# Kernel tuning notes

Measured on AMD Instinct MI355X. Metric: run time of the kernel, lower is better.

The kernel has to match this reference:

```python
import jax, jax.numpy as jnp
import numpy as np

EPS = 1e-08

def setup_inputs() -> dict:
    key = jax.random.key(0)
    k1, k2, k3, k4 = jax.random.split(key, 4)
    batch, n_in, n_out, D = 32768, 256, 512, 16
    x = jax.random.uniform(k1, (batch, n_in), jnp.float32, minval=-1.0, maxval=1.0)
    omega = jax.random.normal(k2, (D, 1), jnp.float32)          # stddev=1.0 init
    phase = 0.1 * jax.random.normal(k3, (D, 1), jnp.float32)    # zeros in module; small noise for non-degenerate test
    std_c = 1.0 / np.sqrt(n_in * D)
    c_basis = std_c * jax.random.normal(k4, (n_out, n_in, D), jnp.float32)
    bias = jnp.zeros((n_out,), jnp.float32)
    return {"x": x, "omega": omega, "phase": phase, "c_basis": c_basis, "bias": bias}

def _basis(x, omega, phase):
    # x: (batch, n_in) -> B: (batch, n_in, D)
    D = omega.shape[0]
    w = omega.reshape(1, 1, D)
    p = phase.reshape(1, 1, D)
    wx = w * x[..., None]
    s = jnp.sin(wx + p)
    mu = jnp.exp(-0.5 * w ** 2) * jnp.sin(p)
    std = jnp.sqrt(0.5 * (1.0 - jnp.exp(-2.0 * w ** 2) * jnp.cos(2.0 * p)) - mu ** 2)
    return (s + mu) / (std + EPS)

def reference(x, omega, phase, c_basis, bias):
    B = _basis(x, omega, phase)                     # (batch, n_in, D)
    y = jnp.einsum('bid,oid->bo', B, c_basis)       # (batch, n_out)
    return y + bias
```

## Files before the change

kernel.cpp:

```cpp
#include <hip/hip_runtime.h>
#include <hip/hip_bf16.h>


#define BATCH 32768
#define NIN   256
#define NOUT  512
#define DDIM  16
#define BM    128
#define BN    512
#define BK    64
#define NKT   ((NIN*DDIM)/BK)
#define TILE_BYTES (BN*BK*2)
#define ABYTES (BM*BK*2)
#define BBYTES (BN*BK*2)
#define EPSV  1e-8f
#define INV2PI 0.15915494309189535f

typedef short  bf16x8 __attribute__((ext_vector_type(8)));
typedef float  f32x4  __attribute__((ext_vector_type(4)));

static __device__ __forceinline__ ushort f2bf(float f) {
  union { __hip_bfloat16 h; ushort u; } cv;
  cv.h = __float2bfloat16(f);
  return cv.u;
}

static __device__ __forceinline__ uint cvt_pk(float lo, float hi) {
  uint r;
  asm("v_cvt_pk_bf16_f32 %0, %1, %2" : "=v"(r) : "v"(lo), "v"(hi));
  return r;
}

static __device__ __forceinline__ float sgpr_f(float v) {
  return __builtin_bit_cast(float,
      __builtin_amdgcn_readfirstlane(__builtin_bit_cast(int, v)));
}

__global__ __launch_bounds__(256) void prep_kernel(
    const float* __restrict__ omega, const float* __restrict__ phase,
    const float* __restrict__ c_basis, const float* __restrict__ bias,
    ushort* __restrict__ cb, float* __restrict__ offs)
{
  __shared__ float s_scale[DDIM];
  __shared__ float s_musc[DDIM];
  __shared__ float s_red[4];

  const int o = blockIdx.x;
  const int t = threadIdx.x;

  if (t < DDIM) {
    float w = omega[t];
    float p = phase[t];
    float mu  = expf(-0.5f * w * w) * sinf(p);
    float var = 0.5f * (1.0f - expf(-2.0f * w * w) * cosf(2.0f * p)) - mu * mu;
    float sd  = sqrtf(fmaxf(var, 0.0f));
    float sc  = 1.0f / (sd + EPSV);
    s_scale[t] = sc;
    s_musc[t]  = mu * sc;
  }
  __syncthreads();

  const float* cp = c_basis + ((size_t)o * NIN + t) * DDIM;
  float cv[DDIM];
  {
    const float4* cp4 = (const float4*)cp;
    float4 a = cp4[0], b = cp4[1], c = cp4[2], d = cp4[3];
    cv[0]=a.x; cv[1]=a.y; cv[2]=a.z; cv[3]=a.w;
    cv[4]=b.x; cv[5]=b.y; cv[6]=b.z; cv[7]=b.w;
    cv[8]=c.x; cv[9]=c.y; cv[10]=c.z; cv[11]=c.w;
    cv[12]=d.x; cv[13]=d.y; cv[14]=d.z; cv[15]=d.w;
  }

  float partial = 0.0f;
  uint pk[8];
#pragma unroll
  for (int d = 0; d < DDIM; d += 2) {
    partial += cv[d] * s_musc[d] + cv[d+1] * s_musc[d+1];
    ushort u0 = f2bf(cv[d]   * s_scale[d]);
    ushort u1 = f2bf(cv[d+1] * s_scale[d+1]);
    pk[d >> 1] = (uint)u0 | ((uint)u1 << 16);
  }

  {
    const int r   = o;
    const int kt  = t >> 2;
    const int swz = (r & 7) << 4;
    char* tile = (char*)cb + (size_t)kt * TILE_BYTES;
    int b0 = r * 128 + (t & 3) * 32;
    *(uint4*)(tile + ((b0     ) ^ swz)) = make_uint4(pk[0], pk[1], pk[2], pk[3]);
    *(uint4*)(tile + ((b0 + 16) ^ swz)) = make_uint4(pk[4], pk[5], pk[6], pk[7]);
  }

#pragma unroll
  for (int off = 32; off > 0; off >>= 1) partial += __shfl_down(partial, off, 64);
  if ((t & 63) == 0) s_red[t >> 6] = partial;
  __syncthreads();
  if (t == 0) offs[o] = bias[o] + s_red[0] + s_red[1] + s_red[2] + s_red[3];
}

__global__ __launch_bounds__(512, 2) void gemm_kernel(
    const float* __restrict__ x, const float* __restrict__ omega,
    const float* __restrict__ phase, const ushort* __restrict__ cb,
    const float* __restrict__ offs, float* __restrict__ out)
{
  extern __shared__ char lds[];

  const int t    = threadIdx.x;
  const int lane = t & 63;
  const int wid  = t >> 6;
  const int wm   = wid >> 2;
  const int wn   = wid & 3;
  const int row0 = blockIdx.x * BM;

  float wv[DDIM], pv[DDIM];
#pragma unroll
  for (int d = 0; d < DDIM; ++d) {
    wv[d] = sgpr_f(omega[d] * INV2PI);
    pv[d] = sgpr_f(phase[d] * INV2PI);
  }

  f32x4 acc[4][8];
#pragma unroll
  for (int m = 0; m < 4; ++m)
#pragma unroll
    for (int n = 0; n < 8; ++n) acc[m][n] = (f32x4){0.f, 0.f, 0.f, 0.f};

  const int arow = t >> 2;
  const int acol = t & 3;
  const float* xbase = x + (size_t)(row0 + arow) * NIN + acol;
  const int aswz = (arow & 7) << 4;
  const int ab0  = arow * 128 + acol * 32;

  const int hi  = lane >> 4;
  const int l15 = lane & 15;

#define GLL(s_, d_) __builtin_amdgcn_global_load_lds(                          \
      (const __attribute__((address_space(1))) void*)(s_),                     \
      (__attribute__((address_space(3))) void*)(d_), 16, 0, 0)

#define ISSUE_B(kt_, sb_)                                                      \
  {                                                                            \
    const char* src = (const char*)cb + (size_t)(kt_) * TILE_BYTES             \
                      + wid * 8192 + lane * 16;                                \
    char* dst = lds + 32768 + (sb_) * BBYTES + wid * 8192;                     \
    GLL(src, dst);                 GLL(src + 1024, dst + 1024);                \
    GLL(src + 2048, dst + 2048);   GLL(src + 3072, dst + 3072);                \
    GLL(src + 4096, dst + 4096);   GLL(src + 5120, dst + 5120);                \
    GLL(src + 6144, dst + 6144);   GLL(src + 7168, dst + 7168);                \
  }

#define SINS_ALL(xx_)                                                          \
    _Pragma("unroll")                                                          \
    for (int d = 0; d < DDIM; d += 2) {                                        \
      float s0 = __builtin_amdgcn_sinf(fmaf(wv[d],   (xx_), pv[d]));           \
      float s1 = __builtin_amdgcn_sinf(fmaf(wv[d+1], (xx_), pv[d+1]));         \
      pk[d >> 1] = cvt_pk(s0, s1);                                             \
    }

#define A_WRITE2(sb_)                                                          \
    *(uint4*)(lds + (sb_) * ABYTES + ((ab0     ) ^ aswz)) =                    \
        make_uint4(pk[0], pk[1], pk[2], pk[3]);                                \
    *(uint4*)(lds + (sb_) * ABYTES + ((ab0 + 16) ^ aswz)) =                    \
        make_uint4(pk[4], pk[5], pk[6], pk[7]);

#define MFMA_HALF(mb_, kk_)                                                    \
  {                                                                            \
    const char* AsB = lds + (mb_) * ABYTES;                                    \
    const char* BsB = lds + 32768 + (mb_) * BBYTES;                            \
    bf16x8 af[4];                                                              \
    _Pragma("unroll")                                                          \
    for (int m = 0; m < 4; ++m) {                                              \
      int rr = wm * 64 + m * 16 + l15;                                         \
      af[m] = *(const bf16x8*)(AsB + ((rr*128 + (kk_)*64 + hi*16) ^ ((rr&7)<<4))); \
    }                                                                          \
    __builtin_amdgcn_s_setprio(1);                                             \
    _Pragma("unroll")                                                          \
    for (int nh = 0; nh < 2; ++nh) {                                           \
      bf16x8 bfr[4];                                                           \
      _Pragma("unroll")                                                        \
      for (int n4 = 0; n4 < 4; ++n4) {                                         \
        int rr = wn * 128 + (nh * 4 + n4) * 16 + l15;                          \
        bfr[n4] = *(const bf16x8*)(BsB + ((rr*128 + (kk_)*64 + hi*16) ^ ((rr&7)<<4))); \
      }                                                                        \
      _Pragma("unroll")                                                        \
      for (int m = 0; m < 4; ++m)                                              \
        _Pragma("unroll")                                                      \
        for (int n4 = 0; n4 < 4; ++n4)                                         \
          acc[m][nh * 4 + n4] = __builtin_amdgcn_mfma_f32_16x16x32_bf16(       \
              af[m], bfr[n4], acc[m][nh * 4 + n4], 0, 0, 0);                   \
    }                                                                          \
    __builtin_amdgcn_s_setprio(0);                                             \
  }

#define CBAR(vm_)                                                              \
  __builtin_amdgcn_sched_barrier(0);                                           \
  asm volatile("s_waitcnt vmcnt(" #vm_ ") lgkmcnt(0)" ::: "memory");           \
  __builtin_amdgcn_s_barrier();                                                \
  __builtin_amdgcn_sched_barrier(0);

#define BODY(kt_, mb_, sb_, XU_, XL_)                                          \
  {                                                                            \
    ISSUE_B(((kt_) + 1 < NKT ? (kt_) + 1 : NKT - 1), sb_);                     \
    XL_ = xbase[((kt_) + 2 < NKT ? (kt_) + 2 : NKT - 1) * 4];                  \
    __builtin_amdgcn_sched_barrier(0);                                         \
    MFMA_HALF(mb_, 0)                                                          \
    __builtin_amdgcn_sched_barrier(0);                                         \
    uint pk[8];                                                                \
    SINS_ALL(XU_)                                                              \
    A_WRITE2(sb_)                                                              \
    __builtin_amdgcn_sched_barrier(0);                                         \
    MFMA_HALF(mb_, 1)                                                          \
    CBAR(1)                                                                    \
  }

  float xs0, xs1;
  {
    float xp = xbase[0];
    __builtin_amdgcn_sched_barrier(0);
    ISSUE_B(0, 0);
    __builtin_amdgcn_sched_barrier(0);
    xs1 = xbase[4];
    __builtin_amdgcn_sched_barrier(0);
    {
      uint pk[8];
      SINS_ALL(xp)
      A_WRITE2(0)
    }
    CBAR(1)
  }

  for (int kt = 0; kt < NKT; kt += 2) {
    BODY(kt,     0, 1, xs1, xs0)
    BODY(kt + 1, 1, 0, xs0, xs1)
  }

#pragma unroll
  for (int n = 0; n < 8; ++n) {
    int col = wn * 128 + n * 16 + l15;
    float off = offs[col];
#pragma unroll
    for (int m = 0; m < 4; ++m) {
      int row = row0 + wm * 64 + m * 16 + hi * 4;
      float* op = out + (size_t)row * NOUT + col;
#pragma unroll
      for (int j = 0; j < 4; ++j)
        op[(size_t)j * NOUT] = acc[m][n][j] + off;
    }
  }
}

extern "C" void kernel_launch(void* const* d_in, const int* in_sizes, int n_in,
                              void* d_out, int out_size, void* d_ws, size_t ws_size,
                              hipStream_t stream) {
  const float* x       = (const float*)d_in[0];
  const float* omega   = (const float*)d_in[1];
  const float* phase   = (const float*)d_in[2];
  const float* c_basis = (const float*)d_in[3];
  const float* bias    = (const float*)d_in[4];
  float* out = (float*)d_out;

  float*  offs = (float*)d_ws;
  ushort* cb   = (ushort*)((char*)d_ws + 2048);

  hipFuncSetAttribute((const void*)gemm_kernel,
                      hipFuncAttributeMaxDynamicSharedMemorySize, 163840);

  prep_kernel<<<NOUT, 256, 0, stream>>>(omega, phase, c_basis, bias, cb, offs);
  gemm_kernel<<<BATCH / BM, 512, 163840, stream>>>(x, omega, phase, cb, offs, out);
}
```

Measured before the change: 127.6 us.

## Stagger MFMA and sine phases between wave groups for ping-pong overlap

Splits the main loop body into two variants selected by wave id. One half of the waves runs all MFMAs first and then the sine/A-tile generation, while the other half does the sine work first and then the MFMAs, all between the same barriers. The goal is to have waves on a SIMD alternate between matrix-core work and VALU transcendental work, so both units stay busy rather than every wave fighting for the same one at once. It adds code size and depends on the hardware actually interleaving the two wave groups.

```diff
diff --git a/kernel.cpp b/kernel.cpp
--- a/kernel.cpp
+++ b/kernel.cpp
@@ -192,23 +192,38 @@
     __builtin_amdgcn_s_setprio(0);                                             \
   }
 
+#define SB __builtin_amdgcn_sched_barrier(0);
+
 #define CBAR(vm_)                                                              \
   __builtin_amdgcn_sched_barrier(0);                                           \
   asm volatile("s_waitcnt vmcnt(" #vm_ ") lgkmcnt(0)" ::: "memory");           \
   __builtin_amdgcn_s_barrier();                                                \
   __builtin_amdgcn_sched_barrier(0);
 
-#define BODY(kt_, mb_, sb_, XU_, XL_)                                          \
+#define BODY_A(kt_, mb_, sb_, XU_, XL_)                                        \
   {                                                                            \
     ISSUE_B(((kt_) + 1 < NKT ? (kt_) + 1 : NKT - 1), sb_);                     \
     XL_ = xbase[((kt_) + 2 < NKT ? (kt_) + 2 : NKT - 1) * 4];                  \
-    __builtin_amdgcn_sched_barrier(0);                                         \
+    SB                                                                         \
     MFMA_HALF(mb_, 0)                                                          \
-    __builtin_amdgcn_sched_barrier(0);                                         \
+    MFMA_HALF(mb_, 1)                                                          \
+    SB                                                                         \
     uint pk[8];                                                                \
     SINS_ALL(XU_)                                                              \
     A_WRITE2(sb_)                                                              \
-    __builtin_amdgcn_sched_barrier(0);                                         \
+    CBAR(1)                                                                    \
+  }
+
+#define BODY_B(kt_, mb_, sb_, XU_, XL_)                                        \
+  {                                                                            \
+    ISSUE_B(((kt_) + 1 < NKT ? (kt_) + 1 : NKT - 1), sb_);                     \
+    XL_ = xbase[((kt_) + 2 < NKT ? (kt_) + 2 : NKT - 1) * 4];                  \
+    SB                                                                         \
+    uint pk[8];                                                                \
+    SINS_ALL(XU_)                                                              \
+    A_WRITE2(sb_)                                                              \
+    SB                                                                         \
+    MFMA_HALF(mb_, 0)                                                          \
     MFMA_HALF(mb_, 1)                                                          \
     CBAR(1)                                                                    \
   }
@@ -216,11 +231,11 @@
   float xs0, xs1;
   {
     float xp = xbase[0];
-    __builtin_amdgcn_sched_barrier(0);
+    SB
     ISSUE_B(0, 0);
-    __builtin_amdgcn_sched_barrier(0);
+    SB
     xs1 = xbase[4];
-    __builtin_amdgcn_sched_barrier(0);
+    SB
     {
       uint pk[8];
       SINS_ALL(xp)
@@ -229,9 +244,16 @@
     CBAR(1)
   }
 
-  for (int kt = 0; kt < NKT; kt += 2) {
-    BODY(kt,     0, 1, xs1, xs0)
-    BODY(kt + 1, 1, 0, xs0, xs1)
+  if (wid & 4) {
+    for (int kt = 0; kt < NKT; kt += 2) {
+      BODY_A(kt,     0, 1, xs1, xs0)
+      BODY_A(kt + 1, 1, 0, xs0, xs1)
+    }
+  } else {
+    for (int kt = 0; kt < NKT; kt += 2) {
+      BODY_B(kt,     0, 1, xs1, xs0)
+      BODY_B(kt + 1, 1, 0, xs0, xs1)
+    }
   }
 
 #pragma unroll
```

Result: slower. 143.6 us (+12.5%).

## Switch GEMM to 32x32x16 bf16 MFMA with matching LDS swizzle layout

Applied to the files above, without the earlier changes.

Replaces the 16x16x32 MFMA tiling (4x8 accumulators per wave) with 32x32x16 MFMA (2x4 accumulators), changing fragment loads, the LDS XOR swizzle for both A and the precomputed B tiles, and the output store mapping. Larger MFMA tiles cut the number of LDS fragment reads per FLOP and may suit the matrix core throughput better. The trade-offs are a different bank-conflict pattern from the new swizzle and a less coalesced output store layout.

```diff
diff --git a/kernel.cpp b/kernel.cpp
--- a/kernel.cpp
+++ b/kernel.cpp
@@ -16,8 +16,8 @@
 #define EPSV  1e-8f
 #define INV2PI 0.15915494309189535f
 
-typedef short  bf16x8 __attribute__((ext_vector_type(8)));
-typedef float  f32x4  __attribute__((ext_vector_type(4)));
+typedef short  bf16x8  __attribute__((ext_vector_type(8)));
+typedef float  f32x16  __attribute__((ext_vector_type(16)));
 
 static __device__ __forceinline__ ushort f2bf(float f) {
   union { __hip_bfloat16 h; ushort u; } cv;
@@ -82,13 +82,14 @@
   }
 
   {
-    const int r   = o;
-    const int kt  = t >> 2;
-    const int swz = (r & 7) << 4;
-    char* tile = (char*)cb + (size_t)kt * TILE_BYTES;
-    int b0 = r * 128 + (t & 3) * 32;
-    *(uint4*)(tile + ((b0     ) ^ swz)) = make_uint4(pk[0], pk[1], pk[2], pk[3]);
-    *(uint4*)(tile + ((b0 + 16) ^ swz)) = make_uint4(pk[4], pk[5], pk[6], pk[7]);
+    const int r  = o;
+    const int kt = t >> 2;
+    const int fo = (r >> 2) & 7;
+    char* tile = (char*)cb + (size_t)kt * TILE_BYTES + r * 128;
+    const int u0 = (2 * (t & 3))     ^ fo;
+    const int u1 = (2 * (t & 3) + 1) ^ fo;
+    *(uint4*)(tile + u0 * 16) = make_uint4(pk[0], pk[1], pk[2], pk[3]);
+    *(uint4*)(tile + u1 * 16) = make_uint4(pk[4], pk[5], pk[6], pk[7]);
   }
 
 #pragma unroll
@@ -119,20 +120,24 @@
     pv[d] = sgpr_f(phase[d] * INV2PI);
   }
 
-  f32x4 acc[4][8];
-#pragma unroll
-  for (int m = 0; m < 4; ++m)
-#pragma unroll
-    for (int n = 0; n < 8; ++n) acc[m][n] = (f32x4){0.f, 0.f, 0.f, 0.f};
+  f32x16 acc[2][4];
+#pragma unroll
+  for (int m = 0; m < 2; ++m)
+#pragma unroll
+    for (int n = 0; n < 4; ++n)
+#pragma unroll
+      for (int j = 0; j < 16; ++j) acc[m][n][j] = 0.f;
 
   const int arow = t >> 2;
   const int acol = t & 3;
   const float* xbase = x + (size_t)(row0 + arow) * NIN + acol;
-  const int aswz = (arow & 7) << 4;
-  const int ab0  = arow * 128 + acol * 32;
-
-  const int hi  = lane >> 4;
-  const int l15 = lane & 15;
+  const int afo  = (arow >> 2) & 7;
+  const int aw0  = arow * 128 + ((2 * acol)     ^ afo) * 16;
+  const int aw1  = arow * 128 + ((2 * acol + 1) ^ afo) * 16;
+
+  const int l31 = lane & 31;
+  const int hi2 = lane >> 5;
+  const int fr  = l31 >> 2;
 
 #define GLL(s_, d_) __builtin_amdgcn_global_load_lds(                          \
       (const __attribute__((address_space(1))) void*)(s_),                     \
@@ -158,39 +163,37 @@
     }
 
 #define A_WRITE2(sb_)                                                          \
-    *(uint4*)(lds + (sb_) * ABYTES + ((ab0     ) ^ aswz)) =                    \
-        make_uint4(pk[0], pk[1], pk[2], pk[3]);                                \
-    *(uint4*)(lds + (sb_) * ABYTES + ((ab0 + 16) ^ aswz)) =                    \
-        make_uint4(pk[4], pk[5], pk[6], pk[7]);
-
-#define MFMA_HALF(mb_, kk_)                                                    \
+    *(uint4*)(lds + (sb_) * ABYTES + aw0) = make_uint4(pk[0], pk[1], pk[2], pk[3]); \
+    *(uint4*)(lds + (sb_) * ABYTES + aw1) = make_uint4(pk[4], pk[5], pk[6], pk[7]);
+
+#define FRAG_OFF(rb_, kk_) (((rb_) + l31) * 128 + (((2 * (kk_) + hi2) ^ fr) * 16))
+
+#define MFMA_2K(mb_, half_)                                                    \
   {                                                                            \
     const char* AsB = lds + (mb_) * ABYTES;                                    \
     const char* BsB = lds + 32768 + (mb_) * BBYTES;                            \
-    bf16x8 af[4];                                                              \
     _Pragma("unroll")                                                          \
-    for (int m = 0; m < 4; ++m) {                                              \
-      int rr = wm * 64 + m * 16 + l15;                                         \
-      af[m] = *(const bf16x8*)(AsB + ((rr*128 + (kk_)*64 + hi*16) ^ ((rr&7)<<4))); \
+    for (int kq = 0; kq < 2; ++kq) {                                           \
+      const int kk = (half_) * 2 + kq;                                         \
+      bf16x8 af[2], bfr[4];                                                    \
+      _Pragma("unroll")                                                        \
+      for (int m = 0; m < 2; ++m)                                              \
+        af[m] = *(const bf16x8*)(AsB + FRAG_OFF(wm * 64 + m * 32, kk));        \
+      _Pragma("unroll")                                                        \
+      for (int n = 0; n < 4; ++n)                                              \
+        bfr[n] = *(const bf16x8*)(BsB + FRAG_OFF(wn * 128 + n * 32, kk));      \
+      __builtin_amdgcn_s_setprio(1);                                           \
+      _Pragma("unroll")                                                        \
+      for (int m = 0; m < 2; ++m)                                              \
+        _Pragma("unroll")                                                      \
+        for (int n = 0; n < 4; ++n)                                            \
+          acc[m][n] = __builtin_amdgcn_mfma_f32_32x32x16_bf16(                 \
+              af[m], bfr[n], acc[m][n], 0, 0, 0);                              \
+      __builtin_amdgcn_s_setprio(0);                                           \
     }                                                                          \
-    __builtin_amdgcn_s_setprio(1);                                             \
-    _Pragma("unroll")                                                          \
-    for (int nh = 0; nh < 2; ++nh) {                                           \
-      bf16x8 bfr[4];                                                           \
-      _Pragma("unroll")                                                        \
-      for (int n4 = 0; n4 < 4; ++n4) {                                         \
-        int rr = wn * 128 + (nh * 4 + n4) * 16 + l15;                          \
-        bfr[n4] = *(const bf16x8*)(BsB + ((rr*128 + (kk_)*64 + hi*16) ^ ((rr&7)<<4))); \
-      }                                                                        \
-      _Pragma("unroll")                                                        \
-      for (int m = 0; m < 4; ++m)                                              \
-        _Pragma("unroll")                                                      \
-        for (int n4 = 0; n4 < 4; ++n4)                                         \
-          acc[m][nh * 4 + n4] = __builtin_amdgcn_mfma_f32_16x16x32_bf16(       \
-              af[m], bfr[n4], acc[m][nh * 4 + n4], 0, 0, 0);                   \
-    }                                                                          \
-    __builtin_amdgcn_s_setprio(0);                                             \
-  }
+  }
+
+#define SB __builtin_amdgcn_sched_barrier(0);
 
 #define CBAR(vm_)                                                              \
   __builtin_amdgcn_sched_barrier(0);                                           \
@@ -202,25 +205,25 @@
   {                                                                            \
     ISSUE_B(((kt_) + 1 < NKT ? (kt_) + 1 : NKT - 1), sb_);                     \
     XL_ = xbase[((kt_) + 2 < NKT ? (kt_) + 2 : NKT - 1) * 4];                  \
-    __builtin_amdgcn_sched_barrier(0);                                         \
-    MFMA_HALF(mb_, 0)                                                          \
-    __builtin_amdgcn_sched_barrier(0);                                         \
+    SB                                                                         \
+    MFMA_2K(mb_, 0)                                                            \
+    SB                                                                         \
     uint pk[8];                                                                \
     SINS_ALL(XU_)                                                              \
     A_WRITE2(sb_)                                                              \
-    __builtin_amdgcn_sched_barrier(0);                                         \
-    MFMA_HALF(mb_, 1)                                                          \
+    SB                                                                         \
+    MFMA_2K(mb_, 1)                                                            \
     CBAR(1)                                                                    \
   }
 
   float xs0, xs1;
   {
     float xp = xbase[0];
-    __builtin_amdgcn_sched_barrier(0);
+    SB
     ISSUE_B(0, 0);
-    __builtin_amdgcn_sched_barrier(0);
+    SB
     xs1 = xbase[4];
-    __builtin_amdgcn_sched_barrier(0);
+    SB
     {
       uint pk[8];
       SINS_ALL(xp)
@@ -235,16 +238,17 @@
   }
 
 #pragma unroll
-  for (int n = 0; n < 8; ++n) {
-    int col = wn * 128 + n * 16 + l15;
+  for (int n = 0; n < 4; ++n) {
+    int col = wn * 128 + n * 32 + l31;
     float off = offs[col];
 #pragma unroll
-    for (int m = 0; m < 4; ++m) {
-      int row = row0 + wm * 64 + m * 16 + hi * 4;
-      float* op = out + (size_t)row * NOUT + col;
-#pragma unroll
-      for (int j = 0; j < 4; ++j)
-        op[(size_t)j * NOUT] = acc[m][n][j] + off;
+    for (int m = 0; m < 2; ++m) {
+      int rbase = row0 + wm * 64 + m * 32 + hi2 * 4;
+#pragma unroll
+      for (int reg = 0; reg < 16; ++reg) {
+        int row = rbase + (reg & 3) + 8 * (reg >> 2);
+        out[(size_t)row * NOUT + col] = acc[m][n][reg] + off;
+      }
     }
   }
 }
```

Result: slower. 146.6 us (+14.9%).
